# Optimization experiments

Hardware: AMD Instinct MI355X
Metric: run time of the kernel (lower is better)

The kernel has to match this reference:

```python
import jax, jax.numpy as jnp
import numpy as np

N = 50000      # nodes
E = 1600000    # edges (before self loops)
IN = 128
OUT = 128
H = 4
HD = OUT // H  # head dim = 32


def setup_inputs() -> dict:
    key = jax.random.key(0)
    k1, k2, k3, k4, k5 = jax.random.split(key, 5)
    x = jax.random.normal(k1, (N, IN), dtype=jnp.float32)
    edge_index = jax.random.randint(k2, (2, E), 0, N, dtype=jnp.int64)
    # xavier-uniform-ish scales
    W = jax.random.normal(k3, (OUT, IN), dtype=jnp.float32) * (1.0 / np.sqrt(IN))
    att_src = jax.random.normal(k4, (1, H, HD), dtype=jnp.float32) * 0.1
    att_dst = jax.random.normal(k5, (1, H, HD), dtype=jnp.float32) * 0.1
    return {"x": x, "edge_index": edge_index, "W": W, "att_src": att_src, "att_dst": att_dst}


def reference(x, edge_index, W, att_src, att_dst):
    n = x.shape[0]
    # add self loops (tg.utils.add_self_loops appends [i, i] edges)
    loops = jnp.arange(n, dtype=edge_index.dtype)
    ei = jnp.concatenate([edge_index, jnp.stack([loops, loops])], axis=1)
    src, dst = ei[0], ei[1]

    # linear projection, split into heads: [n, H, HD]
    h = (x @ W.T).reshape(n, H, HD)

    # per-node attention logits per head: [n, H]
    a_src = jnp.sum(h * att_src, axis=-1)
    a_dst = jnp.sum(h * att_dst, axis=-1)

    # per-edge attention score: gather + leaky_relu
    alpha = a_src[src] + a_dst[dst]                      # [Etot, H]
    alpha = jax.nn.leaky_relu(alpha, negative_slope=0.2)

    # segment softmax grouped by destination node (numerically stable)
    m = jax.ops.segment_max(alpha, dst, num_segments=n)  # [n, H]
    e = jnp.exp(alpha - m[dst])
    s = jax.ops.segment_sum(e, dst, num_segments=n)      # [n, H]
    e = e / s[dst]                                       # [Etot, H]

    # weighted scatter-add aggregation; f_additive adds 1 to the weights
    msg = h[src] * (e[:, :, None] + 1.0)                 # [Etot, H, HD]
    out = jax.ops.segment_sum(msg, dst, num_segments=n)  # [n, H, HD]
    return out.reshape(n, -1)
```

## Files before the change

### kernel.cpp

```cpp
#include <hip/hip_runtime.h>

#define N_NODES 50000
#define E_EDGES 1600000
#define ETOT    (E_EDGES + N_NODES)
#define DIN  128
#define DOUT 128
#define NH   4
#define HD   32

typedef unsigned short ushort_t;
typedef unsigned int uint_t;
typedef __attribute__((ext_vector_type(8))) short bfrag;
typedef __attribute__((ext_vector_type(4))) float ffrag;

__device__ __forceinline__ ushort_t f2bf(float f) {
  uint_t u = __float_as_uint(f);
  u += 0x7fffu + ((u >> 16) & 1u);
  return (ushort_t)(u >> 16);
}
__device__ __forceinline__ float bf_lo(uint_t u) {
  return __uint_as_float(u << 16);
}
__device__ __forceinline__ float bf_hi(uint_t u) {
  return __uint_as_float(u & 0xffff0000u);
}

#define BSZ   64
#define NBUCK ((N_NODES + BSZ - 1) / BSZ)
#define NBP   1024
#define CAP   2560
#define EPB_A 8192
#define NBLK_A ((ETOT + EPB_A - 1) / EPB_A)
#define NCHUNK 13


__global__ __launch_bounds__(256) void binA2_kernel(
    const int* __restrict__ ei, uint_t* __restrict__ ebuf,
    int* __restrict__ cntm, int* __restrict__ offm) {
  __shared__ uint_t lds[EPB_A + NBP + 8];
  uint_t* stage = lds;
  int* hist = (int*)(lds + EPB_A);
  int* wsum = hist + NBP;
  const int tid = threadIdx.x;
  const int cb = blockIdx.x;
  const int e0 = cb * EPB_A;
  const int n = min(EPB_A, ETOT - e0);
  for (int i = tid; i < NBP; i += 256) hist[i] = 0;
  __syncthreads();
  for (int i = tid; i < n; i += 256) {
    int e = e0 + i;
    int si, di;
    if (e < E_EDGES) { si = ei[e]; di = ei[E_EDGES + e]; }
    else             { si = e - E_EDGES; di = si; }
    stage[i] = ((uint_t)di << 16) | (uint_t)si;
    atomicAdd(&hist[di >> 6], 1);
  }
  __syncthreads();
  const int ln = tid & 63, wv = tid >> 6;
  int c0 = hist[4 * tid], c1 = hist[4 * tid + 1];
  int c2 = hist[4 * tid + 2], c3 = hist[4 * tid + 3];
  int p1 = c0, p2 = c0 + c1, p3 = c0 + c1 + c2;
  int tot = p3 + c3;
  int xx = tot;
#pragma unroll
  for (int off = 1; off < 64; off <<= 1) {
    int y = __shfl_up(xx, off, 64);
    if (ln >= off) xx += y;
  }
  if (ln == 63) wsum[wv] = xx;
  __syncthreads();
  if (tid < 4) {
    int w = wsum[tid];
#pragma unroll
    for (int off = 1; off < 4; off <<= 1) {
      int y = __shfl_up(w, off, 64);
      if (tid >= off) w += y;
    }
    wsum[tid] = w;
  }
  __syncthreads();
  const int wo = (wv == 0) ? 0 : wsum[wv - 1];
  const int base = wo + xx - tot;
#pragma unroll
  for (int k = 0; k < 4; k++) {
    int idx = 4 * tid + k;
    int c = k == 0 ? c0 : k == 1 ? c1 : k == 2 ? c2 : c3;
    int o = base + (k == 0 ? 0 : k == 1 ? p1 : k == 2 ? p2 : p3);
    if (idx < NBUCK) {
      cntm[(size_t)cb * NBP + idx] = c;
      offm[(size_t)cb * NBP + idx] = o;
    }
    hist[idx] = o;
  }
  __syncthreads();
  for (int i = tid; i < n; i += 256) {
    uint_t p = stage[i];
    int pos = atomicAdd(&hist[p >> 22], 1);
    if (pos >= 0 && pos < n) ebuf[e0 + pos] = p;
  }
}

__global__ __launch_bounds__(256, 4) void gemm_att_kernel(
    const float* __restrict__ x, const float* __restrict__ W,
    const float* __restrict__ att_src, const float* __restrict__ att_dst,
    ushort_t* __restrict__ hb, float* __restrict__ a_src,
    float* __restrict__ a_dst) {
  __shared__ ushort_t Ws[DIN * DOUT];
  const int tid = threadIdx.x;
  const int gb = blockIdx.x;
  const int wv = tid >> 6, l = tid & 63;
  const int lr = l & 15, lg = l >> 4;
  const int nbase = gb * 64 + wv * 16;
  int na = nbase + lr;
  if (na >= N_NODES) na = N_NODES - 1;
  const float* xrow = x + (size_t)na * DIN;

  float4 px[8];
#pragma unroll
  for (int kt = 0; kt < 4; kt++) {
    px[kt * 2]     = *(const float4*)&xrow[kt * 32 + lg * 8];
    px[kt * 2 + 1] = *(const float4*)&xrow[kt * 32 + lg * 8 + 4];
  }

  for (int u = tid; u < 2048; u += 256) {
    int row = u >> 4;
    float4 w0 = *(const float4*)&W[u * 8];
    float4 w1 = *(const float4*)&W[u * 8 + 4];
    uint4 pk;
    pk.x = (uint_t)f2bf(w0.x) | ((uint_t)f2bf(w0.y) << 16);
    pk.y = (uint_t)f2bf(w0.z) | ((uint_t)f2bf(w0.w) << 16);
    pk.z = (uint_t)f2bf(w1.x) | ((uint_t)f2bf(w1.y) << 16);
    pk.w = (uint_t)f2bf(w1.z) | ((uint_t)f2bf(w1.w) << 16);
    *(uint4*)&Ws[(u ^ (row & 7)) * 8] = pk;
  }
  __syncthreads();

  ffrag acc[8];
#pragma unroll
  for (int oc = 0; oc < 8; oc++) acc[oc] = (ffrag){0.f, 0.f, 0.f, 0.f};

#pragma unroll
  for (int kt = 0; kt < 4; kt++) {
    const float4 x0 = px[kt * 2];
    const float4 x1 = px[kt * 2 + 1];
    bfrag a;
    a[0] = (short)f2bf(x0.x); a[1] = (short)f2bf(x0.y);
    a[2] = (short)f2bf(x0.z); a[3] = (short)f2bf(x0.w);
    a[4] = (short)f2bf(x1.x); a[5] = (short)f2bf(x1.y);
    a[6] = (short)f2bf(x1.z); a[7] = (short)f2bf(x1.w);
#pragma unroll
    for (int oc = 0; oc < 8; oc++) {
      const int u = ((oc * 16 + lr) << 4) + kt * 4 + lg;
      const bfrag b = *(const bfrag*)&Ws[(u ^ (lr & 7)) * 8];
      acc[oc] = __builtin_amdgcn_mfma_f32_16x16x32_bf16(a, b, acc[oc], 0, 0, 0);
    }
  }

#pragma unroll
  for (int oc = 0; oc < 8; oc++) {
#pragma unroll
    for (int j = 0; j < 4; j++) {
      int n = nbase + lg * 4 + j;
      if (n < N_NODES)
        hb[((size_t)n << 7) + oc * 16 + lr] = f2bf(acc[oc][j]);
    }
  }

  float asv[8], adv[8];
#pragma unroll
  for (int oc = 0; oc < 8; oc++) {
    asv[oc] = att_src[oc * 16 + lr];
    adv[oc] = att_dst[oc * 16 + lr];
  }
#pragma unroll
  for (int j = 0; j < 4; j++) {
    float ps[4] = {0.f, 0.f, 0.f, 0.f};
    float pd[4] = {0.f, 0.f, 0.f, 0.f};
#pragma unroll
    for (int oc = 0; oc < 8; oc++) {
      ps[oc >> 1] = fmaf(acc[oc][j], asv[oc], ps[oc >> 1]);
      pd[oc >> 1] = fmaf(acc[oc][j], adv[oc], pd[oc >> 1]);
    }
#pragma unroll
    for (int off = 1; off < 16; off <<= 1) {
#pragma unroll
      for (int hd = 0; hd < 4; hd++) {
        ps[hd] += __shfl_xor(ps[hd], off);
        pd[hd] += __shfl_xor(pd[hd], off);
      }
    }
    int n = nbase + lg * 4 + j;
    if (n < N_NODES && lr < 4) {
      float vs = lr == 0 ? ps[0] : lr == 1 ? ps[1] : lr == 2 ? ps[2] : ps[3];
      float vd = lr == 0 ? pd[0] : lr == 1 ? pd[1] : lr == 2 ? pd[2] : pd[3];
      a_src[n * NH + lr] = vs;
      a_dst[n * NH + lr] = vd;
    }
  }
}

__global__ __launch_bounds__(256) void binB_kernel(
    const uint_t* __restrict__ ebuf, const int* __restrict__ cntm,
    const int* __restrict__ offm,
    int* __restrict__ rs, int* __restrict__ re, int* __restrict__ col) {
  __shared__ uint_t el[CAP];
  __shared__ int cnt_l[BSZ * NCHUNK];
  __shared__ int roff_l[BSZ * NCHUNK];
  __shared__ int wsum[4];
  const int b = blockIdx.x;
  const int tid = threadIdx.x;
  const int ln = tid & 63, wv = tid >> 6;
  const int n0 = b << 6;
  const int nn = min(BSZ, N_NODES - n0);

  int c = (tid < NBLK_A) ? cntm[(size_t)tid * NBP + b] : 0;
  int o = (tid < NBLK_A) ? offm[(size_t)tid * NBP + b] : 0;
  int xx = c;
#pragma unroll
  for (int off = 1; off < 64; off <<= 1) {
    int y = __shfl_up(xx, off, 64);
    if (ln >= off) xx += y;
  }
  if (ln == 63) wsum[wv] = xx;
  __syncthreads();
  if (tid < 4) {
    int w = wsum[tid];
#pragma unroll
    for (int off = 1; off < 4; off <<= 1) {
      int y = __shfl_up(w, off, 64);
      if (tid >= off) w += y;
    }
    wsum[tid] = w;
  }
  __syncthreads();
  const int wo = (wv == 0) ? 0 : wsum[wv - 1];
  const int mystart = wo + xx - c;
  const int total0 = wsum[3];
  const int total = total0 < CAP ? total0 : CAP;
  if (tid < NBLK_A) {
    const uint_t* src = ebuf + (size_t)tid * EPB_A + o;
    for (int j = 0; j < c; j++) {
      int d = mystart + j;
      if (d < CAP) el[d] = src[j];
    }
  }
  for (int k = tid; k < BSZ * NCHUNK; k += 256) cnt_l[k] = 0;
  __syncthreads();

  for (int i = tid; i < total; i += 256) {
    uint_t p = el[i];
    int key = (int)((p >> 16) & 63) * NCHUNK + (int)((p & 0xFFFFu) >> 12);
    atomicAdd(&cnt_l[key], 1);
  }
  __syncthreads();
  if (tid < BSZ) {
    int pref[NCHUNK];
    int tot = 0;
#pragma unroll
    for (int k = 0; k < NCHUNK; k++) { pref[k] = tot; tot += cnt_l[tid * NCHUNK + k]; }
    int x2 = tot;
#pragma unroll
    for (int off = 1; off < 64; off <<= 1) {
      int y = __shfl_up(x2, off, 64);
      if (tid >= off) x2 += y;
    }
    const int nodebase = x2 - tot;
#pragma unroll
    for (int k = 0; k < NCHUNK; k++) roff_l[tid * NCHUNK + k] = nodebase + pref[k];
    if (tid < nn) {
      rs[n0 + tid] = b * CAP + nodebase;
      re[n0 + tid] = b * CAP + nodebase + tot;
    }
  }
  __syncthreads();
  for (int k = tid; k < BSZ * NCHUNK; k += 256) cnt_l[k] = 0;
  __syncthreads();
  for (int i = tid; i < total; i += 256) {
    uint_t p = el[i];
    int si = (int)(p & 0xFFFFu);
    int key = (int)((p >> 16) & 63) * NCHUNK + (si >> 12);
    int pos = atomicAdd(&cnt_l[key], 1);
    int q = b * CAP + roff_l[key] + pos;
    if (q >= 0 && q < NBUCK * CAP) col[q] = si;
  }
}

#define NPB 16
#define CH  16

__global__ __launch_bounds__(256, 8) void agg_kernel(
    const int* __restrict__ col, const int* __restrict__ rs,
    const int* __restrict__ re, const ushort_t* __restrict__ hb,
    const float* __restrict__ a_src, const float* __restrict__ a_dst,
    float* __restrict__ out) {
  __shared__ float w_lds[NPB][CH][NH];
  __shared__ int   si_lds[NPB][CH];
  const int tid  = threadIdx.x;
  const int slot = tid >> 4;
  const int t    = tid & 15;
  const int node = blockIdx.x * NPB + slot;
  const int start = rs[node];
  const int deg   = re[node] - start;
  const float4 ad = *(const float4*)(a_dst + (size_t)node * NH);

  const int head = t >> 2;
  const int c8 = t << 3;
  const ushort_t* hc = hb + c8;
  float s = 0.f;
  float a0 = 0.f, a1 = 0.f, a2 = 0.f, a3 = 0.f;
  float a4 = 0.f, a5 = 0.f, a6 = 0.f, a7 = 0.f;
  float b0 = 0.f, b1 = 0.f, b2 = 0.f, b3 = 0.f;
  float b4 = 0.f, b5 = 0.f, b6 = 0.f, b7 = 0.f;

  int   si_c = 0;
  float4 as_c = make_float4(0.f, 0.f, 0.f, 0.f);
  if (t < deg) {
    si_c = col[start + t];
    si_c = si_c < N_NODES ? si_c : 0;
    as_c = *(const float4*)(a_src + (size_t)si_c * NH);
  }

  for (int base_e = 0; base_e < deg; base_e += CH) {
    int nch = deg - base_e;
    if (nch > CH) nch = CH;
    if (t < nch) {
      si_lds[slot][t] = si_c;
      float v0 = as_c.x + ad.x; v0 = v0 > 0.f ? v0 : 0.2f * v0;
      float v1 = as_c.y + ad.y; v1 = v1 > 0.f ? v1 : 0.2f * v1;
      float v2 = as_c.z + ad.z; v2 = v2 > 0.f ? v2 : 0.2f * v2;
      float v3 = as_c.w + ad.w; v3 = v3 > 0.f ? v3 : 0.2f * v3;
      w_lds[slot][t][0] = __expf(v0);
      w_lds[slot][t][1] = __expf(v1);
      w_lds[slot][t][2] = __expf(v2);
      w_lds[slot][t][3] = __expf(v3);
    }
    __builtin_amdgcn_fence(__ATOMIC_ACQ_REL, "wavefront");
    int nb = base_e + CH;
    if (nb + t < deg) {
      int sn = col[start + nb + t];
      sn = sn < N_NODES ? sn : 0;
      si_c = sn;
      as_c = *(const float4*)(a_src + (size_t)sn * NH);
    }
#pragma unroll 2
    for (int j = 0; j < nch; j++) {
      int si = si_lds[slot][j];
      float e = w_lds[slot][j][head];
      s += e;
      const uint4 hv = *(const uint4*)(hc + ((size_t)si << 7));
      float h0 = bf_lo(hv.x), h1 = bf_hi(hv.x);
      float h2 = bf_lo(hv.y), h3 = bf_hi(hv.y);
      float h4 = bf_lo(hv.z), h5 = bf_hi(hv.z);
      float h6 = bf_lo(hv.w), h7 = bf_hi(hv.w);
      a0 = fmaf(h0, e, a0); b0 += h0;
      a1 = fmaf(h1, e, a1); b1 += h1;
      a2 = fmaf(h2, e, a2); b2 += h2;
      a3 = fmaf(h3, e, a3); b3 += h3;
      a4 = fmaf(h4, e, a4); b4 += h4;
      a5 = fmaf(h5, e, a5); b5 += h5;
      a6 = fmaf(h6, e, a6); b6 += h6;
      a7 = fmaf(h7, e, a7); b7 += h7;
    }
    __builtin_amdgcn_fence(__ATOMIC_ACQ_REL, "wavefront");
  }
  const float inv = 1.0f / s;
  float* op = out + ((size_t)node << 7) + c8;
  *(float4*)(op)     = make_float4(fmaf(a0, inv, b0), fmaf(a1, inv, b1),
                                   fmaf(a2, inv, b2), fmaf(a3, inv, b3));
  *(float4*)(op + 4) = make_float4(fmaf(a4, inv, b4), fmaf(a5, inv, b5),
                                   fmaf(a6, inv, b6), fmaf(a7, inv, b7));
}

extern "C" void kernel_launch(void* const* d_in, const int* in_sizes, int n_in,
                              void* d_out, int out_size, void* d_ws, size_t ws_size,
                              hipStream_t stream) {
  const float* x       = (const float*)d_in[0];
  const int*   ei      = (const int*)d_in[1];
  const float* W       = (const float*)d_in[2];
  const float* att_src = (const float*)d_in[3];
  const float* att_dst = (const float*)d_in[4];
  float* out = (float*)d_out;

  ushort_t* hb = (ushort_t*)d_ws;
  float* a_src = (float*)(hb + (size_t)N_NODES * DOUT);
  float* a_dst = a_src + (size_t)N_NODES * NH;
  int* cntm    = (int*)(a_dst + (size_t)N_NODES * NH);
  int* offm    = cntm + (size_t)NBLK_A * NBP;
  int* rs      = offm + (size_t)NBLK_A * NBP;
  int* re      = rs + N_NODES;
  int* col     = re + N_NODES;
  uint_t* ebuf = (uint_t*)(col + (size_t)NBUCK * CAP);

  binA2_kernel<<<NBLK_A, 256, 0, stream>>>(ei, ebuf, cntm, offm);
  gemm_att_kernel<<<(N_NODES + 63) / 64, 256, 0, stream>>>(
      x, W, att_src, att_dst, hb, a_src, a_dst);
  binB_kernel<<<NBUCK, 256, 0, stream>>>(ebuf, cntm, offm, rs, re, col);
  agg_kernel<<<N_NODES / NPB, 256, 0, stream>>>(col, rs, re, hb, a_src, a_dst, out);
}
```

Baseline: 117.0 us.

## Merge bin/cast and gemm/binB kernels, split attention logits, use 16-bit col indices

Restructures the pipeline. The x and W bf16 casts now run inside the edge-binning kernel as extra blocks, and the GEMM is fused with the bucket-sort binB phase in one launch, with blocks picking their role by index so independent work overlaps. Attention logits move to a separate small kernel that reads back the bf16 h, and col indices shrink to 16 bits to cut aggregation traffic. This adds an extra bf16 x round-trip through memory and computes the logits from rounded h, which changes numerics slightly.

```diff
diff --git a/kernel.cpp b/kernel.cpp
--- a/kernel.cpp
+++ b/kernel.cpp
@@ -32,127 +32,226 @@
 #define EPB_A 8192
 #define NBLK_A ((ETOT + EPB_A - 1) / EPB_A)
 #define NCHUNK 13
-
-
-__global__ __launch_bounds__(256) void binA2_kernel(
+#define CASTX_BLKS 1600
+#define CASTX_F4   1600000
+
+
+__global__ __launch_bounds__(256) void prep_kernel(
     const int* __restrict__ ei, uint_t* __restrict__ ebuf,
-    int* __restrict__ cntm, int* __restrict__ offm) {
+    int* __restrict__ cntm, int* __restrict__ offm,
+    const float* __restrict__ x, ushort_t* __restrict__ xb,
+    const float* __restrict__ W, ushort_t* __restrict__ Wb) {
   __shared__ uint_t lds[EPB_A + NBP + 8];
-  uint_t* stage = lds;
-  int* hist = (int*)(lds + EPB_A);
-  int* wsum = hist + NBP;
   const int tid = threadIdx.x;
-  const int cb = blockIdx.x;
-  const int e0 = cb * EPB_A;
-  const int n = min(EPB_A, ETOT - e0);
-  for (int i = tid; i < NBP; i += 256) hist[i] = 0;
-  __syncthreads();
-  for (int i = tid; i < n; i += 256) {
-    int e = e0 + i;
-    int si, di;
-    if (e < E_EDGES) { si = ei[e]; di = ei[E_EDGES + e]; }
-    else             { si = e - E_EDGES; di = si; }
-    stage[i] = ((uint_t)di << 16) | (uint_t)si;
-    atomicAdd(&hist[di >> 6], 1);
-  }
-  __syncthreads();
-  const int ln = tid & 63, wv = tid >> 6;
-  int c0 = hist[4 * tid], c1 = hist[4 * tid + 1];
-  int c2 = hist[4 * tid + 2], c3 = hist[4 * tid + 3];
-  int p1 = c0, p2 = c0 + c1, p3 = c0 + c1 + c2;
-  int tot = p3 + c3;
-  int xx = tot;
-#pragma unroll
-  for (int off = 1; off < 64; off <<= 1) {
-    int y = __shfl_up(xx, off, 64);
-    if (ln >= off) xx += y;
-  }
-  if (ln == 63) wsum[wv] = xx;
-  __syncthreads();
-  if (tid < 4) {
-    int w = wsum[tid];
-#pragma unroll
-    for (int off = 1; off < 4; off <<= 1) {
-      int y = __shfl_up(w, off, 64);
-      if (tid >= off) w += y;
-    }
-    wsum[tid] = w;
-  }
-  __syncthreads();
-  const int wo = (wv == 0) ? 0 : wsum[wv - 1];
-  const int base = wo + xx - tot;
+
+  if (blockIdx.x < NBLK_A) {
+    uint_t* stage = lds;
+    int* hist = (int*)(lds + EPB_A);
+    int* wsum = hist + NBP;
+    const int cb = blockIdx.x;
+    const int e0 = cb * EPB_A;
+    const int n = min(EPB_A, ETOT - e0);
+    for (int i = tid; i < NBP; i += 256) hist[i] = 0;
+    __syncthreads();
+    for (int i = tid; i < n; i += 256) {
+      int e = e0 + i;
+      int si, di;
+      if (e < E_EDGES) { si = ei[e]; di = ei[E_EDGES + e]; }
+      else             { si = e - E_EDGES; di = si; }
+      stage[i] = ((uint_t)di << 16) | (uint_t)si;
+      atomicAdd(&hist[di >> 6], 1);
+    }
+    __syncthreads();
+    const int ln = tid & 63, wv = tid >> 6;
+    int c0 = hist[4 * tid], c1 = hist[4 * tid + 1];
+    int c2 = hist[4 * tid + 2], c3 = hist[4 * tid + 3];
+    int p1 = c0, p2 = c0 + c1, p3 = c0 + c1 + c2;
+    int tot = p3 + c3;
+    int xx = tot;
+#pragma unroll
+    for (int off = 1; off < 64; off <<= 1) {
+      int y = __shfl_up(xx, off, 64);
+      if (ln >= off) xx += y;
+    }
+    if (ln == 63) wsum[wv] = xx;
+    __syncthreads();
+    if (tid < 4) {
+      int w = wsum[tid];
+#pragma unroll
+      for (int off = 1; off < 4; off <<= 1) {
+        int y = __shfl_up(w, off, 64);
+        if (tid >= off) w += y;
+      }
+      wsum[tid] = w;
+    }
+    __syncthreads();
+    const int wo = (wv == 0) ? 0 : wsum[wv - 1];
+    const int base = wo + xx - tot;
+#pragma unroll
+    for (int k = 0; k < 4; k++) {
+      int idx = 4 * tid + k;
+      int c = k == 0 ? c0 : k == 1 ? c1 : k == 2 ? c2 : c3;
+      int o = base + (k == 0 ? 0 : k == 1 ? p1 : k == 2 ? p2 : p3);
+      if (idx < NBUCK) {
+        cntm[(size_t)cb * NBP + idx] = c;
+        offm[(size_t)cb * NBP + idx] = o;
+      }
+      hist[idx] = o;
+    }
+    __syncthreads();
+    for (int i = tid; i < n; i += 256) {
+      uint_t p = stage[i];
+      int pos = atomicAdd(&hist[p >> 22], 1);
+      if (pos >= 0 && pos < n) ebuf[e0 + pos] = p;
+    }
+    return;
+  }
+
+  if (blockIdx.x < NBLK_A + CASTX_BLKS) {
+    const int idx = (blockIdx.x - NBLK_A) * 256 + tid;
+#pragma unroll
+    for (int k = 0; k < 4; k++) {
+      int i = idx + k * (CASTX_BLKS * 256);
+      if (i < CASTX_F4) {
+        float4 v = ((const float4*)x)[i];
+        ushort4 o;
+        o.x = f2bf(v.x); o.y = f2bf(v.y); o.z = f2bf(v.z); o.w = f2bf(v.w);
+        ((ushort4*)xb)[i] = o;
+      }
+    }
+    return;
+  }
+
+  const int idx = (blockIdx.x - NBLK_A - CASTX_BLKS) * 256 + tid;
 #pragma unroll
   for (int k = 0; k < 4; k++) {
-    int idx = 4 * tid + k;
-    int c = k == 0 ? c0 : k == 1 ? c1 : k == 2 ? c2 : c3;
-    int o = base + (k == 0 ? 0 : k == 1 ? p1 : k == 2 ? p2 : p3);
-    if (idx < NBUCK) {
-      cntm[(size_t)cb * NBP + idx] = c;
-      offm[(size_t)cb * NBP + idx] = o;
-    }
-    hist[idx] = o;
-  }
-  __syncthreads();
-  for (int i = tid; i < n; i += 256) {
-    uint_t p = stage[i];
-    int pos = atomicAdd(&hist[p >> 22], 1);
-    if (pos >= 0 && pos < n) ebuf[e0 + pos] = p;
-  }
-}
-
-__global__ __launch_bounds__(256, 4) void gemm_att_kernel(
-    const float* __restrict__ x, const float* __restrict__ W,
-    const float* __restrict__ att_src, const float* __restrict__ att_dst,
-    ushort_t* __restrict__ hb, float* __restrict__ a_src,
-    float* __restrict__ a_dst) {
+    int i = idx + k * 1024;
+    if (i < DIN * DOUT / 4) {
+      float4 v = ((const float4*)W)[i];
+      ushort4 o;
+      o.x = f2bf(v.x); o.y = f2bf(v.y); o.z = f2bf(v.z); o.w = f2bf(v.w);
+      ((ushort4*)Wb)[i] = o;
+    }
+  }
+}
+
+__global__ __launch_bounds__(256, 4) void gemm_binB_kernel(
+    const uint_t* __restrict__ ebuf, const int* __restrict__ cntm,
+    const int* __restrict__ offm, int* __restrict__ rs, int* __restrict__ re,
+    ushort_t* __restrict__ col,
+    const ushort_t* __restrict__ xb, const ushort_t* __restrict__ Wb,
+    ushort_t* __restrict__ hb) {
   __shared__ ushort_t Ws[DIN * DOUT];
   const int tid = threadIdx.x;
-  const int gb = blockIdx.x;
+
+  if (blockIdx.x < NBUCK) {
+    uint_t* el  = (uint_t*)&Ws[0];
+    int* cnt_l  = (int*)&Ws[CAP * 2];
+    int* roff_l = cnt_l + BSZ * NCHUNK;
+    int* wsum   = roff_l + BSZ * NCHUNK;
+    const int b = blockIdx.x;
+    const int ln = tid & 63, wv = tid >> 6;
+    const int n0 = b << 6;
+    const int nn = min(BSZ, N_NODES - n0);
+
+    int c = (tid < NBLK_A) ? cntm[(size_t)tid * NBP + b] : 0;
+    int o = (tid < NBLK_A) ? offm[(size_t)tid * NBP + b] : 0;
+    int xx = c;
+#pragma unroll
+    for (int off = 1; off < 64; off <<= 1) {
+      int y = __shfl_up(xx, off, 64);
+      if (ln >= off) xx += y;
+    }
+    if (ln == 63) wsum[wv] = xx;
+    __syncthreads();
+    if (tid < 4) {
+      int w = wsum[tid];
+#pragma unroll
+      for (int off = 1; off < 4; off <<= 1) {
+        int y = __shfl_up(w, off, 64);
+        if (tid >= off) w += y;
+      }
+      wsum[tid] = w;
+    }
+    __syncthreads();
+    const int wo = (wv == 0) ? 0 : wsum[wv - 1];
+    const int mystart = wo + xx - c;
+    const int total0 = wsum[3];
+    const int total = total0 < CAP ? total0 : CAP;
+    if (tid < NBLK_A) {
+      const uint_t* src = ebuf + (size_t)tid * EPB_A + o;
+      for (int j = 0; j < c; j++) {
+        int d = mystart + j;
+        if (d < CAP) el[d] = src[j];
+      }
+    }
+    for (int k = tid; k < BSZ * NCHUNK; k += 256) cnt_l[k] = 0;
+    __syncthreads();
+
+    for (int i = tid; i < total; i += 256) {
+      uint_t p = el[i];
+      int key = (int)((p >> 16) & 63) * NCHUNK + (int)((p & 0xFFFFu) >> 12);
+      atomicAdd(&cnt_l[key], 1);
+    }
+    __syncthreads();
+    if (tid < BSZ) {
+      int pref[NCHUNK];
+      int tot = 0;
+#pragma unroll
+      for (int k = 0; k < NCHUNK; k++) { pref[k] = tot; tot += cnt_l[tid * NCHUNK + k]; }
+      int x2 = tot;
+#pragma unroll
+      for (int off = 1; off < 64; off <<= 1) {
+        int y = __shfl_up(x2, off, 64);
+        if (tid >= off) x2 += y;
+      }
+      const int nodebase = x2 - tot;
+#pragma unroll
+      for (int k = 0; k < NCHUNK; k++) roff_l[tid * NCHUNK + k] = nodebase + pref[k];
+      if (tid < nn) {
+        rs[n0 + tid] = b * CAP + nodebase;
+        re[n0 + tid] = b * CAP + nodebase + tot;
+      }
+    }
+    __syncthreads();
+    for (int k = tid; k < BSZ * NCHUNK; k += 256) cnt_l[k] = 0;
+    __syncthreads();
+    for (int i = tid; i < total; i += 256) {
+      uint_t p = el[i];
+      int si = (int)(p & 0xFFFFu);
+      int key = (int)((p >> 16) & 63) * NCHUNK + (si >> 12);
+      int pos = atomicAdd(&cnt_l[key], 1);
+      int q = b * CAP + roff_l[key] + pos;
+      if (q >= 0 && q < NBUCK * CAP) col[q] = (ushort_t)si;
+    }
+    return;
+  }
+
+  const int gb = blockIdx.x - NBUCK;
+  for (int u = tid; u < 2048; u += 256) {
+    int row = u >> 4;
+    *(uint4*)&Ws[(u ^ (row & 7)) * 8] = *(const uint4*)&Wb[u * 8];
+  }
+  __syncthreads();
+
   const int wv = tid >> 6, l = tid & 63;
   const int lr = l & 15, lg = l >> 4;
   const int nbase = gb * 64 + wv * 16;
   int na = nbase + lr;
   if (na >= N_NODES) na = N_NODES - 1;
-  const float* xrow = x + (size_t)na * DIN;
-
-  float4 px[8];
+
+  ffrag acc[8];
+#pragma unroll
+  for (int oc = 0; oc < 8; oc++) acc[oc] = (ffrag){0.f, 0.f, 0.f, 0.f};
+
 #pragma unroll
   for (int kt = 0; kt < 4; kt++) {
-    px[kt * 2]     = *(const float4*)&xrow[kt * 32 + lg * 8];
-    px[kt * 2 + 1] = *(const float4*)&xrow[kt * 32 + lg * 8 + 4];
-  }
-
-  for (int u = tid; u < 2048; u += 256) {
-    int row = u >> 4;
-    float4 w0 = *(const float4*)&W[u * 8];
-    float4 w1 = *(const float4*)&W[u * 8 + 4];
-    uint4 pk;
-    pk.x = (uint_t)f2bf(w0.x) | ((uint_t)f2bf(w0.y) << 16);
-    pk.y = (uint_t)f2bf(w0.z) | ((uint_t)f2bf(w0.w) << 16);
-    pk.z = (uint_t)f2bf(w1.x) | ((uint_t)f2bf(w1.y) << 16);
-    pk.w = (uint_t)f2bf(w1.z) | ((uint_t)f2bf(w1.w) << 16);
-    *(uint4*)&Ws[(u ^ (row & 7)) * 8] = pk;
-  }
-  __syncthreads();
-
-  ffrag acc[8];
-#pragma unroll
-  for (int oc = 0; oc < 8; oc++) acc[oc] = (ffrag){0.f, 0.f, 0.f, 0.f};
-
-#pragma unroll
-  for (int kt = 0; kt < 4; kt++) {
-    const float4 x0 = px[kt * 2];
-    const float4 x1 = px[kt * 2 + 1];
-    bfrag a;
-    a[0] = (short)f2bf(x0.x); a[1] = (short)f2bf(x0.y);
-    a[2] = (short)f2bf(x0.z); a[3] = (short)f2bf(x0.w);
-    a[4] = (short)f2bf(x1.x); a[5] = (short)f2bf(x1.y);
-    a[6] = (short)f2bf(x1.z); a[7] = (short)f2bf(x1.w);
+    const bfrag a = *(const bfrag*)&xb[((size_t)na << 7) + kt * 32 + lg * 8];
 #pragma unroll
     for (int oc = 0; oc < 8; oc++) {
       const int u = ((oc * 16 + lr) << 4) + kt * 4 + lg;
-      const bfrag b = *(const bfrag*)&Ws[(u ^ (lr & 7)) * 8];
-      acc[oc] = __builtin_amdgcn_mfma_f32_16x16x32_bf16(a, b, acc[oc], 0, 0, 0);
+      const bfrag bfr = *(const bfrag*)&Ws[(u ^ (lr & 7)) * 8];
+      acc[oc] = __builtin_amdgcn_mfma_f32_16x16x32_bf16(a, bfr, acc[oc], 0, 0, 0);
     }
   }
 
@@ -165,131 +264,42 @@
         hb[((size_t)n << 7) + oc * 16 + lr] = f2bf(acc[oc][j]);
     }
   }
-
-  float asv[8], adv[8];
-#pragma unroll
-  for (int oc = 0; oc < 8; oc++) {
-    asv[oc] = att_src[oc * 16 + lr];
-    adv[oc] = att_dst[oc * 16 + lr];
-  }
-#pragma unroll
-  for (int j = 0; j < 4; j++) {
-    float ps[4] = {0.f, 0.f, 0.f, 0.f};
-    float pd[4] = {0.f, 0.f, 0.f, 0.f};
-#pragma unroll
-    for (int oc = 0; oc < 8; oc++) {
-      ps[oc >> 1] = fmaf(acc[oc][j], asv[oc], ps[oc >> 1]);
-      pd[oc >> 1] = fmaf(acc[oc][j], adv[oc], pd[oc >> 1]);
-    }
-#pragma unroll
-    for (int off = 1; off < 16; off <<= 1) {
-#pragma unroll
-      for (int hd = 0; hd < 4; hd++) {
-        ps[hd] += __shfl_xor(ps[hd], off);
-        pd[hd] += __shfl_xor(pd[hd], off);
-      }
-    }
-    int n = nbase + lg * 4 + j;
-    if (n < N_NODES && lr < 4) {
-      float vs = lr == 0 ? ps[0] : lr == 1 ? ps[1] : lr == 2 ? ps[2] : ps[3];
-      float vd = lr == 0 ? pd[0] : lr == 1 ? pd[1] : lr == 2 ? pd[2] : pd[3];
-      a_src[n * NH + lr] = vs;
-      a_dst[n * NH + lr] = vd;
-    }
-  }
-}
-
-__global__ __launch_bounds__(256) void binB_kernel(
-    const uint_t* __restrict__ ebuf, const int* __restrict__ cntm,
-    const int* __restrict__ offm,
-    int* __restrict__ rs, int* __restrict__ re, int* __restrict__ col) {
-  __shared__ uint_t el[CAP];
-  __shared__ int cnt_l[BSZ * NCHUNK];
-  __shared__ int roff_l[BSZ * NCHUNK];
-  __shared__ int wsum[4];
-  const int b = blockIdx.x;
-  const int tid = threadIdx.x;
-  const int ln = tid & 63, wv = tid >> 6;
-  const int n0 = b << 6;
-  const int nn = min(BSZ, N_NODES - n0);
-
-  int c = (tid < NBLK_A) ? cntm[(size_t)tid * NBP + b] : 0;
-  int o = (tid < NBLK_A) ? offm[(size_t)tid * NBP + b] : 0;
-  int xx = c;
-#pragma unroll
-  for (int off = 1; off < 64; off <<= 1) {
-    int y = __shfl_up(xx, off, 64);
-    if (ln >= off) xx += y;
-  }
-  if (ln == 63) wsum[wv] = xx;
-  __syncthreads();
-  if (tid < 4) {
-    int w = wsum[tid];
-#pragma unroll
-    for (int off = 1; off < 4; off <<= 1) {
-      int y = __shfl_up(w, off, 64);
-      if (tid >= off) w += y;
-    }
-    wsum[tid] = w;
-  }
-  __syncthreads();
-  const int wo = (wv == 0) ? 0 : wsum[wv - 1];
-  const int mystart = wo + xx - c;
-  const int total0 = wsum[3];
-  const int total = total0 < CAP ? total0 : CAP;
-  if (tid < NBLK_A) {
-    const uint_t* src = ebuf + (size_t)tid * EPB_A + o;
-    for (int j = 0; j < c; j++) {
-      int d = mystart + j;
-      if (d < CAP) el[d] = src[j];
-    }
-  }
-  for (int k = tid; k < BSZ * NCHUNK; k += 256) cnt_l[k] = 0;
-  __syncthreads();
-
-  for (int i = tid; i < total; i += 256) {
-    uint_t p = el[i];
-    int key = (int)((p >> 16) & 63) * NCHUNK + (int)((p & 0xFFFFu) >> 12);
-    atomicAdd(&cnt_l[key], 1);
-  }
-  __syncthreads();
-  if (tid < BSZ) {
-    int pref[NCHUNK];
-    int tot = 0;
-#pragma unroll
-    for (int k = 0; k < NCHUNK; k++) { pref[k] = tot; tot += cnt_l[tid * NCHUNK + k]; }
-    int x2 = tot;
-#pragma unroll
-    for (int off = 1; off < 64; off <<= 1) {
-      int y = __shfl_up(x2, off, 64);
-      if (tid >= off) x2 += y;
-    }
-    const int nodebase = x2 - tot;
-#pragma unroll
-    for (int k = 0; k < NCHUNK; k++) roff_l[tid * NCHUNK + k] = nodebase + pref[k];
-    if (tid < nn) {
-      rs[n0 + tid] = b * CAP + nodebase;
-      re[n0 + tid] = b * CAP + nodebase + tot;
-    }
-  }
-  __syncthreads();
-  for (int k = tid; k < BSZ * NCHUNK; k += 256) cnt_l[k] = 0;
-  __syncthreads();
-  for (int i = tid; i < total; i += 256) {
-    uint_t p = el[i];
-    int si = (int)(p & 0xFFFFu);
-    int key = (int)((p >> 16) & 63) * NCHUNK + (si >> 12);
-    int pos = atomicAdd(&cnt_l[key], 1);
-    int q = b * CAP + roff_l[key] + pos;
-    if (q >= 0 && q < NBUCK * CAP) col[q] = si;
-  }
+}
+
+__global__ __launch_bounds__(256) void att_logits_kernel(
+    const ushort_t* __restrict__ hb, const float* __restrict__ att_src,
+    const float* __restrict__ att_dst, float* __restrict__ a_src,
+    float* __restrict__ a_dst) {
+  int t = blockIdx.x * 256 + threadIdx.x;
+  if (t >= N_NODES * NH) return;
+  int n = t >> 2, hd = t & 3;
+  const uint4* hp = (const uint4*)(hb + ((size_t)n << 7) + (hd << 5));
+  const float* as = att_src + (hd << 5);
+  const float* ad = att_dst + (hd << 5);
+  float s1 = 0.f, s2 = 0.f;
+#pragma unroll
+  for (int q = 0; q < 4; q++) {
+    uint4 hv = hp[q];
+    float c0 = bf_lo(hv.x), c1 = bf_hi(hv.x);
+    float c2 = bf_lo(hv.y), c3 = bf_hi(hv.y);
+    float c4 = bf_lo(hv.z), c5 = bf_hi(hv.z);
+    float c6 = bf_lo(hv.w), c7 = bf_hi(hv.w);
+    float4 a0 = *(const float4*)(as + q * 8);
+    float4 a1 = *(const float4*)(as + q * 8 + 4);
+    float4 d0 = *(const float4*)(ad + q * 8);
+    float4 d1 = *(const float4*)(ad + q * 8 + 4);
+    s1 += c0*a0.x + c1*a0.y + c2*a0.z + c3*a0.w + c4*a1.x + c5*a1.y + c6*a1.z + c7*a1.w;
+    s2 += c0*d0.x + c1*d0.y + c2*d0.z + c3*d0.w + c4*d1.x + c5*d1.y + c6*d1.z + c7*d1.w;
+  }
+  a_src[t] = s1;
+  a_dst[t] = s2;
 }
 
 #define NPB 16
 #define CH  16
 
 __global__ __launch_bounds__(256, 8) void agg_kernel(
-    const int* __restrict__ col, const int* __restrict__ rs,
+    const ushort_t* __restrict__ col, const int* __restrict__ rs,
     const int* __restrict__ re, const ushort_t* __restrict__ hb,
     const float* __restrict__ a_src, const float* __restrict__ a_dst,
     float* __restrict__ out) {
@@ -382,18 +392,22 @@
   float* out = (float*)d_out;
 
   ushort_t* hb = (ushort_t*)d_ws;
-  float* a_src = (float*)(hb + (size_t)N_NODES * DOUT);
+  ushort_t* xb = hb + (size_t)N_NODES * DOUT;
+  ushort_t* Wb = xb + (size_t)N_NODES * DIN;
+  float* a_src = (float*)(Wb + DIN * DOUT);
   float* a_dst = a_src + (size_t)N_NODES * NH;
   int* cntm    = (int*)(a_dst + (size_t)N_NODES * NH);
   int* offm    = cntm + (size_t)NBLK_A * NBP;
   int* rs      = offm + (size_t)NBLK_A * NBP;
   int* re      = rs + N_NODES;
-  int* col     = re + N_NODES;
+  ushort_t* col = (ushort_t*)(re + N_NODES);
   uint_t* ebuf = (uint_t*)(col + (size_t)NBUCK * CAP);
 
-  binA2_kernel<<<NBLK_A, 256, 0, stream>>>(ei, ebuf, cntm, offm);
-  gemm_att_kernel<<<(N_NODES + 63) / 64, 256, 0, stream>>>(
-      x, W, att_src, att_dst, hb, a_src, a_dst);
-  binB_kernel<<<NBUCK, 256, 0, stream>>>(ebuf, cntm, offm, rs, re, col);
+  prep_kernel<<<NBLK_A + CASTX_BLKS + 4, 256, 0, stream>>>(
+      ei, ebuf, cntm, offm, x, xb, W, Wb);
+  gemm_binB_kernel<<<NBUCK + (N_NODES + 63) / 64, 256, 0, stream>>>(
+      ebuf, cntm, offm, rs, re, col, xb, Wb, hb);
+  att_logits_kernel<<<(N_NODES * NH + 255) / 256, 256, 0, stream>>>(
+      hb, att_src, att_dst, a_src, a_dst);
   agg_kernel<<<N_NODES / NPB, 256, 0, stream>>>(col, rs, re, hb, a_src, a_dst, out);
 }
```

Result: faster. 112.6 us (-3.8%).
